# Optimization experiments

Hardware: AMD Instinct MI355X
Metric: run time of the kernel (lower is better)

## Reference

```python
import jax, jax.numpy as jnp
import numpy as np

N_NODES = 50000
HID = 64
EPS = 1e-5
POS_COLS = np.array([0, 1, 14])  # pos_x, pos_y, battery


def setup_inputs() -> dict:
    key = jax.random.key(0)
    ks = jax.random.split(key, 10)
    x = jax.random.normal(ks[0], (N_NODES, 16), dtype=jnp.float32)
    edge_index = jax.random.randint(ks[1], (2, 1600000), 0, N_NODES, dtype=jnp.int64)
    # 6 structurally identical conv layers: Linear(6,64) -> ReLU -> Linear(64,64)
    W1 = jax.random.normal(ks[2], (6, 6, HID), dtype=jnp.float32) * (1.0 / np.sqrt(6))
    b1 = jax.random.normal(ks[3], (6, HID), dtype=jnp.float32) * 0.02
    W2 = jax.random.normal(ks[4], (6, HID, HID), dtype=jnp.float32) * (1.0 / np.sqrt(HID))
    b2 = jax.random.normal(ks[5], (6, HID), dtype=jnp.float32) * 0.02
    # 5 BatchNorm layers (training mode: batch statistics over nodes)
    bn_gamma = jnp.ones((5, HID), dtype=jnp.float32) + 0.1 * jax.random.normal(ks[6], (5, HID), dtype=jnp.float32)
    bn_beta = 0.1 * jax.random.normal(ks[7], (5, HID), dtype=jnp.float32)
    return {"x": x, "edge_index": edge_index, "W1": W1, "b1": b1,
            "W2": W2, "b2": b2, "bn_gamma": bn_gamma, "bn_beta": bn_beta}


def _conv(x, src, dst, W1, b1, W2, b2):
    # pos_battery = x[:, [0,1,14]]; message = MLP(cat(x_j - x_i, x_i)); aggr='add' at target i
    p = x[:, POS_COLS]                       # [N, 3]
    x_i = p[dst]                             # targets  [E, 3]
    x_j = p[src]                             # sources  [E, 3]
    m = jnp.concatenate([x_j - x_i, x_i], axis=1)   # [E, 6]
    h = jax.nn.relu(m @ W1 + b1) @ W2 + b2          # [E, HID]
    return jax.ops.segment_sum(h, dst, num_segments=x.shape[0])


def _bn(h, gamma, beta):
    mu = jnp.mean(h, axis=0)
    var = jnp.var(h, axis=0)  # biased, matching BatchNorm training normalization
    return (h - mu) * jax.lax.rsqrt(var + EPS) * gamma + beta


def reference(x, edge_index, W1, b1, W2, b2, bn_gamma, bn_beta):
    n = x.shape[0]
    loop = jnp.arange(n, dtype=edge_index.dtype)
    src = jnp.concatenate([edge_index[0], loop])   # add_self_loops (done per layer in torch,
    dst = jnp.concatenate([edge_index[1], loop])   # identical result every layer)
    h = x
    for l in range(6):
        h = _conv(h, src, dst, W1[l], b1[l], W2[l], b2[l])
        if l < 5:
            h = jax.nn.relu(_bn(h, bn_gamma[l], bn_beta[l]))
    return h
```

## Files before the change

kernel.cpp:

```cpp
#include <hip/hip_runtime.h>
#include <hip/hip_fp16.h>
#include <cstdint>

#define NN 50000
#define NQBLK 12500
#define NGBLK 12500
#define EPSV 1e-5f

#define NPB 128
#define BSH 7
#define NBKT 391
#define CHUNK 4096
#define EPT 16
#define LDSE 6144

#define NSLOT 128

typedef unsigned short ushort_t;
typedef _Float16 half2v __attribute__((ext_vector_type(2)));

__global__ __launch_bounds__(256) void k_hist1(const int* __restrict__ dst, int E, int nchunk,
                                               int* __restrict__ hist, float* __restrict__ gsumsp) {
    __shared__ int cnt[NBKT];
    int t = threadIdx.x, blk = blockIdx.x;
    if (blk == 0) {
        for (int z = t; z < 5 * NSLOT * 8; z += 256) gsumsp[z] = 0.f;
    }
    for (int b = t; b < NBKT; b += 256) cnt[b] = 0;
    __syncthreads();
    int base = blk * CHUNK;
#pragma unroll
    for (int k = 0; k < EPT; ++k) {
        int e = base + k * 256 + t;
        if (e < E) atomicAdd(&cnt[dst[e] >> BSH], 1);
    }
    __syncthreads();
    for (int b = t; b < NBKT; b += 256) hist[(size_t)b * nchunk + blk] = cnt[b];
}

__global__ __launch_bounds__(256) void k_scanA(const int* __restrict__ in, int n,
                                               int* __restrict__ presum, int* __restrict__ blocksum) {
    __shared__ int lds[256];
    int t = threadIdx.x, g = blockIdx.x * 256 + t;
    int v = (g < n) ? in[g] : 0;
    lds[t] = v;
    __syncthreads();
    for (int off = 1; off < 256; off <<= 1) {
        int x = (t >= off) ? lds[t - off] : 0;
        __syncthreads();
        lds[t] += x;
        __syncthreads();
    }
    if (g < n) presum[g] = lds[t];
    if (t == 255) blocksum[blockIdx.x] = lds[255];
}

__global__ __launch_bounds__(256) void k_scanB(const int* __restrict__ blocksum,
                                               int nb, int* __restrict__ blockoff) {
    __shared__ int lds[256];
    __shared__ int carry_s;
    int t = threadIdx.x;
    if (t == 0) carry_s = 0;
    __syncthreads();
    for (int base = 0; base < nb; base += 256) {
        int g = base + t;
        int v = (g < nb) ? blocksum[g] : 0;
        lds[t] = v;
        __syncthreads();
        for (int off = 1; off < 256; off <<= 1) {
            int x = (t >= off) ? lds[t - off] : 0;
            __syncthreads();
            lds[t] += x;
            __syncthreads();
        }
        if (g < nb) blockoff[g] = lds[t] - v + carry_s;
        __syncthreads();
        if (t == 255) carry_s += lds[255];
        __syncthreads();
    }
}

__global__ __launch_bounds__(256) void k_scanC(const int* __restrict__ presum,
                                               const int* __restrict__ hist,
                                               const int* __restrict__ blockoff,
                                               int n, int nchunk, int* __restrict__ offsT) {
    int g = blockIdx.x * 256 + threadIdx.x;
    if (g < n) {
        int val = presum[g] - hist[g] + blockoff[blockIdx.x];
        int b = g / nchunk;
        int c = g - b * nchunk;
        offsT[(size_t)c * NBKT + b] = val;
    }
}

__global__ __launch_bounds__(256) void k_scatter1(const int* __restrict__ src,
                                                  const int* __restrict__ dst, int E,
                                                  const int* __restrict__ offsT,
                                                  int* __restrict__ ebuf) {
    __shared__ int pos[NBKT];
    int t = threadIdx.x, blk = blockIdx.x;
    for (int b = t; b < NBKT; b += 256) pos[b] = offsT[(size_t)blk * NBKT + b];
    __syncthreads();
    int base = blk * CHUNK;
#pragma unroll
    for (int k = 0; k < EPT; ++k) {
        int e = base + k * 256 + t;
        if (e < E) {
            int d = dst[e];
            int b = d >> BSH;
            int p = atomicAdd(&pos[b], 1);
            ebuf[p] = ((d & (NPB - 1)) << 16) | src[e];
        }
    }
}

__global__ __launch_bounds__(256) void k_bucket_csr(const int* __restrict__ ebuf,
                                                    const int* __restrict__ offsT, int E,
                                                    int* __restrict__ rowstart,
                                                    ushort_t* __restrict__ colsrc) {
    __shared__ int cnt[NPB];
    __shared__ int s[NPB];
    __shared__ int pos2[NPB];
    __shared__ ushort_t lout[LDSE];
    int t = threadIdx.x, b = blockIdx.x;
    int bstart = offsT[b];
    int bend = (b + 1 < NBKT) ? offsT[b + 1] : E;
    int m = bend - bstart;
    if (t < NPB) cnt[t] = 0;
    __syncthreads();
    for (int i = bstart + t; i < bend; i += 256) atomicAdd(&cnt[ebuf[i] >> 16], 1);
    __syncthreads();
    if (t < NPB) s[t] = cnt[t];
    __syncthreads();
    for (int off = 1; off < NPB; off <<= 1) {
        int x = (t < NPB && t >= off) ? s[t - off] : 0;
        __syncthreads();
        if (t < NPB) s[t] += x;
        __syncthreads();
    }
    if (t < NPB) {
        int excl = s[t] - cnt[t];
        int node = b * NPB + t;
        if (node < NN) rowstart[node] = bstart + excl;
        pos2[t] = excl;
    }
    __syncthreads();
    if (m <= LDSE) {
        for (int i = bstart + t; i < bend; i += 256) {
            int v = ebuf[i];
            int p = atomicAdd(&pos2[v >> 16], 1);
            lout[p] = (ushort_t)(v & 0xFFFF);
        }
        __syncthreads();
        for (int i = t; i < m; i += 256) colsrc[bstart + i] = lout[i];
    } else {
        for (int i = bstart + t; i < bend; i += 256) {
            int v = ebuf[i];
            int p = atomicAdd(&pos2[v >> 16], 1);
            colsrc[bstart + p] = (ushort_t)(v & 0xFFFF);
        }
    }
    if (b == NBKT - 1 && t == 0) rowstart[NN] = E;
}

__global__ __launch_bounds__(256) void k_q(
    const float* __restrict__ pin, int pstride, int c0, int c1, int c2,
    const float* __restrict__ W1l, const float* __restrict__ b1l,
    const float* __restrict__ scale, const float* __restrict__ shift, int use_bn,
    __half* __restrict__ qs, __half* __restrict__ qd) {
    int idx = blockIdx.x * 256 + threadIdx.x;
    int v = idx >> 6, c = idx & 63;
    const float* prow = pin + (size_t)v * pstride;
    float p0 = prow[c0], p1 = prow[c1], p2 = prow[c2];
    if (use_bn) {
        p0 = fmaxf(0.f, p0 * scale[0] + shift[0]);
        p1 = fmaxf(0.f, p1 * scale[1] + shift[1]);
        p2 = fmaxf(0.f, p2 * scale[2] + shift[2]);
    }
    float w0 = W1l[0 * 64 + c], w1 = W1l[1 * 64 + c], w2 = W1l[2 * 64 + c];
    float w3 = W1l[3 * 64 + c], w4 = W1l[4 * 64 + c], w5 = W1l[5 * 64 + c];
    qs[idx] = __float2half(p0 * w0 + p1 * w1 + p2 * w2);
    qd[idx] = __float2half(p0 * (w3 - w0) + p1 * (w4 - w1) + p2 * (w5 - w2) + b1l[c]);
}

__device__ __forceinline__ half2v bitcast_h2(unsigned int u) {
    union { unsigned int u; half2v h; } cvt;
    cvt.u = u;
    return cvt.h;
}

__device__ __forceinline__ void accum8f(const char* __restrict__ qsb, unsigned int byteoff,
                                        const half2v qd2[4], float acc[8]) {
    uint4 q = *reinterpret_cast<const uint4*>(qsb + byteoff);
    unsigned int wd[4] = {q.x, q.y, q.z, q.w};
    const half2v z2 = {(_Float16)0.0f, (_Float16)0.0f};
#pragma unroll
    for (int d = 0; d < 4; ++d) {
        half2v r = bitcast_h2(wd[d]) + qd2[d];
        r = __builtin_elementwise_max(r, z2);
        acc[2 * d]     += (float)r.x;
        acc[2 * d + 1] += (float)r.y;
    }
}

__device__ __forceinline__ void edge_loop(const char* __restrict__ qsb,
                                          const ushort_t* __restrict__ colsrc,
                                          int start, int end, int es, int cg,
                                          const half2v qd2[4], float acc[8]) {
    int lane = (es << 3) | cg;
    unsigned int cg16 = (unsigned int)(cg << 4);
    const half2v z2 = {(_Float16)0.0f, (_Float16)0.0f};
    int i = start;
    while (i < end) {
        int cnt = min(64, end - i);
        int sl = (lane < cnt) ? (int)colsrc[i + lane] : 0;
        uint4 q[8];
#pragma unroll
        for (int k = 0; k < 8; ++k) {
            int s = __shfl(sl, (k << 3) + es);
            q[k] = *reinterpret_cast<const uint4*>(qsb + (((unsigned int)(s << 7)) | cg16));
        }
        half2v h[4] = {z2, z2, z2, z2};
#pragma unroll
        for (int k = 0; k < 8; ++k) {
            bool ok = ((k << 3) + es) < cnt;
            unsigned int wd[4] = {q[k].x, q[k].y, q[k].z, q[k].w};
#pragma unroll
            for (int d = 0; d < 4; ++d) {
                half2v r = bitcast_h2(wd[d]) + qd2[d];
                r = __builtin_elementwise_max(r, z2);
                h[d] += ok ? r : z2;
            }
        }
#pragma unroll
        for (int d = 0; d < 4; ++d) {
            acc[2 * d]     += (float)h[d].x;
            acc[2 * d + 1] += (float)h[d].y;
        }
        i += cnt;
    }
}

__global__ __launch_bounds__(256) void k_gather3(
    const __half* __restrict__ qs, const __half* __restrict__ qd,
    const int* __restrict__ rowstart, const ushort_t* __restrict__ colsrc,
    const float* __restrict__ W2l, const float* __restrict__ b2l,
    float* __restrict__ pnext, float* __restrict__ gsum_l) {
    __shared__ float w2c[3][64];
    __shared__ float b2c[3];
    __shared__ float part[4][8];
    int tid = threadIdx.x;
    if (tid < 192) {
        int cj = tid >> 6;
        int col = (cj == 0) ? 0 : ((cj == 1) ? 1 : 14);
        w2c[cj][tid & 63] = W2l[(tid & 63) * 64 + col];
    }
    if (tid < 3) b2c[tid] = b2l[(tid == 0) ? 0 : ((tid == 1) ? 1 : 14)];
    __syncthreads();

    int w = tid >> 6, lane = tid & 63;
    int es = lane >> 3, cg = lane & 7;
    int v = blockIdx.x * 4 + w;
    const char* qsb = (const char*)qs;
    uint4 qq = ((const uint4*)qd)[(size_t)v * 8 + cg];
    unsigned int qw[4] = {qq.x, qq.y, qq.z, qq.w};
    half2v qd2[4];
#pragma unroll
    for (int d = 0; d < 4; ++d) qd2[d] = bitcast_h2(qw[d]);

    float acc[8] = {0, 0, 0, 0, 0, 0, 0, 0};
    int start = rowstart[v], end = rowstart[v + 1];
    if (es == 0) accum8f(qsb, ((unsigned int)(v << 7)) | (cg << 4), qd2, acc);
    edge_loop(qsb, colsrc, start, end, es, cg, qd2, acc);

#pragma unroll
    for (int k = 0; k < 8; ++k) {
        acc[k] += __shfl_xor(acc[k], 8);
        acc[k] += __shfl_xor(acc[k], 16);
        acc[k] += __shfl_xor(acc[k], 32);
    }
    float degp1 = (float)(end - start + 1);
#pragma unroll
    for (int j = 0; j < 3; ++j) {
        float t = 0.f;
#pragma unroll
        for (int k = 0; k < 8; ++k) t += acc[k] * w2c[j][cg * 8 + k];
        t += __shfl_xor(t, 1);
        t += __shfl_xor(t, 2);
        t += __shfl_xor(t, 4);
        if (lane == 0) {
            float val = t + degp1 * b2c[j];
            pnext[v * 3 + j] = val;
            part[w][j] = val;
            part[w][3 + j] = val * val;
        }
    }
    __syncthreads();
    if (tid < 6) {
        float ssum = part[0][tid] + part[1][tid] + part[2][tid] + part[3][tid];
        atomicAdd(&gsum_l[(blockIdx.x & (NSLOT - 1)) * 8 + tid], ssum);
    }
}

__global__ void k_bnfin(const float* __restrict__ gs,
                        const float* __restrict__ gamma_l, const float* __restrict__ beta_l,
                        float* __restrict__ scale, float* __restrict__ shift) {
    __shared__ float red[6][8];
    __shared__ float tot[6];
    int t = threadIdx.x;
    int j = t >> 3, k = t & 7;
    if (j < 6) {
        float s = 0.f;
        for (int slot = k; slot < NSLOT; slot += 8) s += gs[slot * 8 + j];
        red[j][k] = s;
    }
    __syncthreads();
    if (t < 6) {
        float s = 0.f;
#pragma unroll
        for (int k2 = 0; k2 < 8; ++k2) s += red[t][k2];
        tot[t] = s;
    }
    __syncthreads();
    if (t < 3) {
        const int cols[3] = {0, 1, 14};
        float mu = tot[t] / (float)NN;
        float var = tot[t + 3] / (float)NN - mu * mu;
        float rs = rsqrtf(var + EPSV);
        float g = gamma_l[cols[t]];
        scale[t] = rs * g;
        shift[t] = beta_l[cols[t]] - mu * rs * g;
    }
}

__global__ __launch_bounds__(256) void k_gather_full(
    const __half* __restrict__ qs, const __half* __restrict__ qd,
    const int* __restrict__ rowstart, const ushort_t* __restrict__ colsrc,
    const float* __restrict__ W2l, const float* __restrict__ b2l,
    float* __restrict__ out) {
    __shared__ float lds[4][64];
    int tid = threadIdx.x;
    int w = tid >> 6, lane = tid & 63;
    int es = lane >> 3, cg = lane & 7;
    int v = blockIdx.x * 4 + w;
    const char* qsb = (const char*)qs;
    uint4 qq = ((const uint4*)qd)[(size_t)v * 8 + cg];
    unsigned int qw[4] = {qq.x, qq.y, qq.z, qq.w};
    half2v qd2[4];
#pragma unroll
    for (int d = 0; d < 4; ++d) qd2[d] = bitcast_h2(qw[d]);

    float acc[8] = {0, 0, 0, 0, 0, 0, 0, 0};
    int start = rowstart[v], end = rowstart[v + 1];
    if (es == 0) accum8f(qsb, ((unsigned int)(v << 7)) | (cg << 4), qd2, acc);
    edge_loop(qsb, colsrc, start, end, es, cg, qd2, acc);

#pragma unroll
    for (int k = 0; k < 8; ++k) {
        acc[k] += __shfl_xor(acc[k], 8);
        acc[k] += __shfl_xor(acc[k], 16);
        acc[k] += __shfl_xor(acc[k], 32);
    }
    if (es == 0) {
#pragma unroll
        for (int k = 0; k < 8; ++k) lds[w][cg * 8 + k] = acc[k];
    }
    __syncthreads();
    float degp1 = (float)(end - start + 1);
    float sum = degp1 * b2l[lane];
    for (int k = 0; k < 64; ++k) sum += lds[w][k] * W2l[k * 64 + lane];
    out[(size_t)v * 64 + lane] = sum;
}


static inline size_t align_up(size_t x) { return (x + 255) & ~(size_t)255; }

extern "C" void kernel_launch(void* const* d_in, const int* in_sizes, int n_in,
                              void* d_out, int out_size, void* d_ws, size_t ws_size,
                              hipStream_t stream) {
    const float* x     = (const float*)d_in[0];
    const int*   ei    = (const int*)d_in[1];
    const float* W1    = (const float*)d_in[2];
    const float* b1    = (const float*)d_in[3];
    const float* W2    = (const float*)d_in[4];
    const float* b2    = (const float*)d_in[5];
    const float* gamma = (const float*)d_in[6];
    const float* beta  = (const float*)d_in[7];
    float* out = (float*)d_out;
    const int E = in_sizes[1] / 2;
    const int* src = ei;
    const int* dst = ei + E;

    const int nchunk = (E + CHUNK - 1) / CHUNK;
    const int nscan  = NBKT * nchunk;
    const int nsb    = (nscan + 255) / 256;

    char* base = (char*)d_ws;
    size_t off = 0;
    __half* qs = (__half*)(base + off);     off = align_up(off + (size_t)NN * 64 * 2);
    __half* qd = (__half*)(base + off);     off = align_up(off + (size_t)NN * 64 * 2);
    float* pA = (float*)(base + off);       off = align_up(off + (size_t)NN * 3 * 4);
    float* pB = (float*)(base + off);       off = align_up(off + (size_t)NN * 3 * 4);
    int* rowstart = (int*)(base + off);     off = align_up(off + (size_t)(NN + 1) * 4);
    ushort_t* colsrc = (ushort_t*)(base + off); off = align_up(off + (size_t)E * 2);
    int* ebuf     = (int*)(base + off);     off = align_up(off + (size_t)E * 4);
    int* hist     = (int*)(base + off);     off = align_up(off + (size_t)nscan * 4);
    int* offsT    = (int*)(base + off);     off = align_up(off + (size_t)nscan * 4);
    int* presum   = (int*)(base + off);     off = align_up(off + (size_t)nscan * 4);
    int* bsum     = (int*)(base + off);     off = align_up(off + (size_t)nsb * 4);
    int* boff     = (int*)(base + off);     off = align_up(off + (size_t)nsb * 4);
    float* gsumsp = (float*)(base + off);   off = align_up(off + (size_t)5 * NSLOT * 8 * 4);
    float* scale  = (float*)(base + off);   off = align_up(off + 64 * 4);
    float* shift  = (float*)(base + off);   off = align_up(off + 64 * 4);
    (void)ws_size; (void)n_in; (void)out_size;

    k_hist1<<<nchunk, 256, 0, stream>>>(dst, E, nchunk, hist, gsumsp);
    k_scanA<<<nsb, 256, 0, stream>>>(hist, nscan, presum, bsum);
    k_scanB<<<1, 256, 0, stream>>>(bsum, nsb, boff);
    k_scanC<<<nsb, 256, 0, stream>>>(presum, hist, boff, nscan, nchunk, offsT);
    k_scatter1<<<nchunk, 256, 0, stream>>>(src, dst, E, offsT, ebuf);
    k_bucket_csr<<<NBKT, 256, 0, stream>>>(ebuf, offsT, E, rowstart, colsrc);

    float* pc = pA;
    float* pn = pB;
    for (int l = 0; l < 6; ++l) {
        const float* pin = (l == 0) ? x : pc;
        int pstride = (l == 0) ? 16 : 3;
        int c0 = 0, c1 = 1, c2 = (l == 0) ? 14 : 2;
        k_q<<<NQBLK, 256, 0, stream>>>(pin, pstride, c0, c1, c2,
                                       W1 + (size_t)l * 6 * 64, b1 + (size_t)l * 64,
                                       scale, shift, (l > 0) ? 1 : 0, qs, qd);
        if (l < 5) {
            k_gather3<<<NGBLK, 256, 0, stream>>>(qs, qd, rowstart, colsrc,
                                                 W2 + (size_t)l * 64 * 64, b2 + (size_t)l * 64,
                                                 pn, gsumsp + (size_t)l * NSLOT * 8);
            k_bnfin<<<1, 64, 0, stream>>>(gsumsp + (size_t)l * NSLOT * 8,
                                          gamma + (size_t)l * 64, beta + (size_t)l * 64,
                                          scale, shift);
            float* tmp = pc; pc = pn; pn = tmp;
        } else {
            k_gather_full<<<NGBLK, 256, 0, stream>>>(qs, qd, rowstart, colsrc,
                                                     W2 + (size_t)5 * 64 * 64, b2 + (size_t)5 * 64,
                                                     out);
        }
    }
}
```

Before: 459.6 us.

## Split gather into channel-half passes with half-split q layout and separate projection

Stores qs/qd as two 32-channel halves (planar by half) so each gather pass touches a 3.2MB table per half, improving cache locality of random source reads. The gather runs as 2x blocks, each processing 16 edges per wave-iteration with full-64 fast path and templated tails, writing fp32 hsum to a new buffer. W2 projection and BN partial sums move to separate lightweight kernels reading hsum. Adds an extra 12.8MB write/read per layer and doubles colsrc/rowstart reads in exchange for better L2 hit rate.

```diff
diff --git a/kernel.cpp b/kernel.cpp
--- a/kernel.cpp
+++ b/kernel.cpp
@@ -18,6 +18,8 @@
 
 typedef unsigned short ushort_t;
 typedef _Float16 half2v __attribute__((ext_vector_type(2)));
+typedef unsigned int uintv4 __attribute__((ext_vector_type(4)));
+typedef float floatv4 __attribute__((ext_vector_type(4)));
 
 __global__ __launch_bounds__(256) void k_hist1(const int* __restrict__ dst, int E, int nchunk,
                                                int* __restrict__ hist, float* __restrict__ gsumsp) {
@@ -179,8 +181,9 @@
     }
     float w0 = W1l[0 * 64 + c], w1 = W1l[1 * 64 + c], w2 = W1l[2 * 64 + c];
     float w3 = W1l[3 * 64 + c], w4 = W1l[4 * 64 + c], w5 = W1l[5 * 64 + c];
-    qs[idx] = __float2half(p0 * w0 + p1 * w1 + p2 * w2);
-    qd[idx] = __float2half(p0 * (w3 - w0) + p1 * (w4 - w1) + p2 * (w5 - w2) + b1l[c]);
+    size_t o = (size_t)(c >> 5) * NN * 32 + (size_t)v * 32 + (c & 31);
+    qs[o] = __float2half(p0 * w0 + p1 * w1 + p2 * w2);
+    qd[o] = __float2half(p0 * (w3 - w0) + p1 * (w4 - w1) + p2 * (w5 - w2) + b1l[c]);
 }
 
 __device__ __forceinline__ half2v bitcast_h2(unsigned int u) {
@@ -189,61 +192,131 @@
     return cvt.h;
 }
 
-__device__ __forceinline__ void accum8f(const char* __restrict__ qsb, unsigned int byteoff,
-                                        const half2v qd2[4], float acc[8]) {
-    uint4 q = *reinterpret_cast<const uint4*>(qsb + byteoff);
-    unsigned int wd[4] = {q.x, q.y, q.z, q.w};
+__device__ __forceinline__ void edge_full64(const char* __restrict__ qsb,
+                                            const ushort_t* __restrict__ colsrc,
+                                            int i, int lane, int es, unsigned int cg16,
+                                            const half2v qd2[4], float acc[8]) {
     const half2v z2 = {(_Float16)0.0f, (_Float16)0.0f};
+    int sl = (int)__builtin_nontemporal_load(colsrc + i + lane);
+    uint4 q[4];
+#pragma unroll
+    for (int k = 0; k < 4; ++k) {
+        int s = __shfl(sl, (k << 4) + es);
+        q[k] = *reinterpret_cast<const uint4*>(qsb + (((unsigned int)(s << 6)) | cg16));
+    }
+    half2v h[4] = {z2, z2, z2, z2};
+#pragma unroll
+    for (int k = 0; k < 4; ++k) {
+        unsigned int wd[4] = {q[k].x, q[k].y, q[k].z, q[k].w};
+#pragma unroll
+        for (int d = 0; d < 4; ++d) {
+            half2v r = bitcast_h2(wd[d]) + qd2[d];
+            r = __builtin_elementwise_max(r, z2);
+            h[d] += r;
+        }
+    }
 #pragma unroll
     for (int d = 0; d < 4; ++d) {
-        half2v r = bitcast_h2(wd[d]) + qd2[d];
-        r = __builtin_elementwise_max(r, z2);
-        acc[2 * d]     += (float)r.x;
-        acc[2 * d + 1] += (float)r.y;
-    }
-}
-
-__device__ __forceinline__ void edge_loop(const char* __restrict__ qsb,
+        acc[2 * d]     += (float)h[d].x;
+        acc[2 * d + 1] += (float)h[d].y;
+    }
+}
+
+template <int NL>
+__device__ __forceinline__ void edge_tail(const char* __restrict__ qsb,
                                           const ushort_t* __restrict__ colsrc,
-                                          int start, int end, int es, int cg,
+                                          int i, int r, int lane, int es, unsigned int cg16,
                                           const half2v qd2[4], float acc[8]) {
-    int lane = (es << 3) | cg;
+    const half2v z2 = {(_Float16)0.0f, (_Float16)0.0f};
+    int sl = (lane < r) ? (int)__builtin_nontemporal_load(colsrc + i + lane) : 0;
+    uint4 q[NL];
+#pragma unroll
+    for (int k = 0; k < NL; ++k) {
+        int s = __shfl(sl, (k << 4) + es);
+        q[k] = *reinterpret_cast<const uint4*>(qsb + (((unsigned int)(s << 6)) | cg16));
+    }
+    half2v h[4] = {z2, z2, z2, z2};
+#pragma unroll
+    for (int k = 0; k < NL; ++k) {
+        bool ok = ((k << 4) + es) < r;
+        unsigned int wd[4] = {q[k].x, q[k].y, q[k].z, q[k].w};
+#pragma unroll
+        for (int d = 0; d < 4; ++d) {
+            half2v t = bitcast_h2(wd[d]) + qd2[d];
+            t = __builtin_elementwise_max(t, z2);
+            h[d] += ok ? t : z2;
+        }
+    }
+#pragma unroll
+    for (int d = 0; d < 4; ++d) {
+        acc[2 * d]     += (float)h[d].x;
+        acc[2 * d + 1] += (float)h[d].y;
+    }
+}
+
+__global__ __launch_bounds__(256) void k_gatherA(
+    const __half* __restrict__ qsh, const __half* __restrict__ qdh,
+    const int* __restrict__ rowstart, const ushort_t* __restrict__ colsrc,
+    float* __restrict__ hsum) {
+    int tid = threadIdx.x;
+    int w = tid >> 6, lane = tid & 63;
+    int es = lane >> 2, cg = lane & 3;
     unsigned int cg16 = (unsigned int)(cg << 4);
-    const half2v z2 = {(_Float16)0.0f, (_Float16)0.0f};
+    int bb = blockIdx.x;
+    int half = (bb >= NGBLK) ? 1 : 0;
+    int v = (bb - half * NGBLK) * 4 + w;
+    const char* qsb = (const char*)qsh + (size_t)half * NN * 64;
+    const char* qdb = (const char*)qdh + (size_t)half * NN * 64;
+
+    uintv4 qq = __builtin_nontemporal_load(
+        reinterpret_cast<const uintv4*>(qdb + ((size_t)v << 6)) + cg);
+    unsigned int qw[4] = {qq.x, qq.y, qq.z, qq.w};
+    half2v qd2[4];
+#pragma unroll
+    for (int d = 0; d < 4; ++d) qd2[d] = bitcast_h2(qw[d]);
+
+    float acc[8] = {0, 0, 0, 0, 0, 0, 0, 0};
+    int start = rowstart[v], end = rowstart[v + 1];
+
+    if (es == 0) {
+        const half2v z2 = {(_Float16)0.0f, (_Float16)0.0f};
+        uint4 q = *reinterpret_cast<const uint4*>(qsb + (((unsigned int)(v << 6)) | cg16));
+        unsigned int wd[4] = {q.x, q.y, q.z, q.w};
+#pragma unroll
+        for (int d = 0; d < 4; ++d) {
+            half2v r = bitcast_h2(wd[d]) + qd2[d];
+            r = __builtin_elementwise_max(r, z2);
+            acc[2 * d]     += (float)r.x;
+            acc[2 * d + 1] += (float)r.y;
+        }
+    }
+
     int i = start;
-    while (i < end) {
-        int cnt = min(64, end - i);
-        int sl = (lane < cnt) ? (int)colsrc[i + lane] : 0;
-        uint4 q[8];
-#pragma unroll
-        for (int k = 0; k < 8; ++k) {
-            int s = __shfl(sl, (k << 3) + es);
-            q[k] = *reinterpret_cast<const uint4*>(qsb + (((unsigned int)(s << 7)) | cg16));
-        }
-        half2v h[4] = {z2, z2, z2, z2};
-#pragma unroll
-        for (int k = 0; k < 8; ++k) {
-            bool ok = ((k << 3) + es) < cnt;
-            unsigned int wd[4] = {q[k].x, q[k].y, q[k].z, q[k].w};
-#pragma unroll
-            for (int d = 0; d < 4; ++d) {
-                half2v r = bitcast_h2(wd[d]) + qd2[d];
-                r = __builtin_elementwise_max(r, z2);
-                h[d] += ok ? r : z2;
-            }
-        }
-#pragma unroll
-        for (int d = 0; d < 4; ++d) {
-            acc[2 * d]     += (float)h[d].x;
-            acc[2 * d + 1] += (float)h[d].y;
-        }
-        i += cnt;
-    }
-}
-
-__global__ __launch_bounds__(256) void k_gather3(
-    const __half* __restrict__ qs, const __half* __restrict__ qd,
-    const int* __restrict__ rowstart, const ushort_t* __restrict__ colsrc,
+    while (end - i >= 64) { edge_full64(qsb, colsrc, i, lane, es, cg16, qd2, acc); i += 64; }
+    int r = end - i;
+    if      (r > 48) edge_tail<4>(qsb, colsrc, i, r, lane, es, cg16, qd2, acc);
+    else if (r > 32) edge_tail<3>(qsb, colsrc, i, r, lane, es, cg16, qd2, acc);
+    else if (r > 16) edge_tail<2>(qsb, colsrc, i, r, lane, es, cg16, qd2, acc);
+    else if (r > 0)  edge_tail<1>(qsb, colsrc, i, r, lane, es, cg16, qd2, acc);
+
+#pragma unroll
+    for (int k = 0; k < 8; ++k) {
+        acc[k] += __shfl_xor(acc[k], 4);
+        acc[k] += __shfl_xor(acc[k], 8);
+        acc[k] += __shfl_xor(acc[k], 16);
+        acc[k] += __shfl_xor(acc[k], 32);
+    }
+    if (es == 0) {
+        floatv4 a0 = {acc[0], acc[1], acc[2], acc[3]};
+        floatv4 a1 = {acc[4], acc[5], acc[6], acc[7]};
+        floatv4* dst = reinterpret_cast<floatv4*>(hsum + (size_t)v * 64 + half * 32 + cg * 8);
+        __builtin_nontemporal_store(a0, dst);
+        __builtin_nontemporal_store(a1, dst + 1);
+    }
+}
+
+__global__ __launch_bounds__(256) void k_proj3(
+    const float* __restrict__ hsum, const int* __restrict__ rowstart,
     const float* __restrict__ W2l, const float* __restrict__ b2l,
     float* __restrict__ pnext, float* __restrict__ gsum_l) {
     __shared__ float w2c[3][64];
@@ -259,35 +332,19 @@
     __syncthreads();
 
     int w = tid >> 6, lane = tid & 63;
-    int es = lane >> 3, cg = lane & 7;
     int v = blockIdx.x * 4 + w;
-    const char* qsb = (const char*)qs;
-    uint4 qq = ((const uint4*)qd)[(size_t)v * 8 + cg];
-    unsigned int qw[4] = {qq.x, qq.y, qq.z, qq.w};
-    half2v qd2[4];
-#pragma unroll
-    for (int d = 0; d < 4; ++d) qd2[d] = bitcast_h2(qw[d]);
-
-    float acc[8] = {0, 0, 0, 0, 0, 0, 0, 0};
+    float hv = __builtin_nontemporal_load(hsum + (size_t)v * 64 + lane);
     int start = rowstart[v], end = rowstart[v + 1];
-    if (es == 0) accum8f(qsb, ((unsigned int)(v << 7)) | (cg << 4), qd2, acc);
-    edge_loop(qsb, colsrc, start, end, es, cg, qd2, acc);
-
-#pragma unroll
-    for (int k = 0; k < 8; ++k) {
-        acc[k] += __shfl_xor(acc[k], 8);
-        acc[k] += __shfl_xor(acc[k], 16);
-        acc[k] += __shfl_xor(acc[k], 32);
-    }
     float degp1 = (float)(end - start + 1);
 #pragma unroll
     for (int j = 0; j < 3; ++j) {
-        float t = 0.f;
-#pragma unroll
-        for (int k = 0; k < 8; ++k) t += acc[k] * w2c[j][cg * 8 + k];
+        float t = hv * w2c[j][lane];
         t += __shfl_xor(t, 1);
         t += __shfl_xor(t, 2);
         t += __shfl_xor(t, 4);
+        t += __shfl_xor(t, 8);
+        t += __shfl_xor(t, 16);
+        t += __shfl_xor(t, 32);
         if (lane == 0) {
             float val = t + degp1 * b2c[j];
             pnext[v * 3 + j] = val;
@@ -333,39 +390,18 @@
     }
 }
 
-__global__ __launch_bounds__(256) void k_gather_full(
-    const __half* __restrict__ qs, const __half* __restrict__ qd,
-    const int* __restrict__ rowstart, const ushort_t* __restrict__ colsrc,
+__global__ __launch_bounds__(256) void k_projfull(
+    const float* __restrict__ hsum, const int* __restrict__ rowstart,
     const float* __restrict__ W2l, const float* __restrict__ b2l,
     float* __restrict__ out) {
     __shared__ float lds[4][64];
     int tid = threadIdx.x;
     int w = tid >> 6, lane = tid & 63;
-    int es = lane >> 3, cg = lane & 7;
     int v = blockIdx.x * 4 + w;
-    const char* qsb = (const char*)qs;
-    uint4 qq = ((const uint4*)qd)[(size_t)v * 8 + cg];
-    unsigned int qw[4] = {qq.x, qq.y, qq.z, qq.w};
-    half2v qd2[4];
-#pragma unroll
-    for (int d = 0; d < 4; ++d) qd2[d] = bitcast_h2(qw[d]);
-
-    float acc[8] = {0, 0, 0, 0, 0, 0, 0, 0};
+    float hv = __builtin_nontemporal_load(hsum + (size_t)v * 64 + lane);
+    lds[w][lane] = hv;
+    __syncthreads();
     int start = rowstart[v], end = rowstart[v + 1];
-    if (es == 0) accum8f(qsb, ((unsigned int)(v << 7)) | (cg << 4), qd2, acc);
-    edge_loop(qsb, colsrc, start, end, es, cg, qd2, acc);
-
-#pragma unroll
-    for (int k = 0; k < 8; ++k) {
-        acc[k] += __shfl_xor(acc[k], 8);
-        acc[k] += __shfl_xor(acc[k], 16);
-        acc[k] += __shfl_xor(acc[k], 32);
-    }
-    if (es == 0) {
-#pragma unroll
-        for (int k = 0; k < 8; ++k) lds[w][cg * 8 + k] = acc[k];
-    }
-    __syncthreads();
     float degp1 = (float)(end - start + 1);
     float sum = degp1 * b2l[lane];
     for (int k = 0; k < 64; ++k) sum += lds[w][k] * W2l[k * 64 + lane];
@@ -399,6 +435,7 @@
     size_t off = 0;
     __half* qs = (__half*)(base + off);     off = align_up(off + (size_t)NN * 64 * 2);
     __half* qd = (__half*)(base + off);     off = align_up(off + (size_t)NN * 64 * 2);
+    float* hsum = (float*)(base + off);     off = align_up(off + (size_t)NN * 64 * 4);
     float* pA = (float*)(base + off);       off = align_up(off + (size_t)NN * 3 * 4);
     float* pB = (float*)(base + off);       off = align_up(off + (size_t)NN * 3 * 4);
     int* rowstart = (int*)(base + off);     off = align_up(off + (size_t)(NN + 1) * 4);
@@ -430,18 +467,19 @@
         k_q<<<NQBLK, 256, 0, stream>>>(pin, pstride, c0, c1, c2,
                                        W1 + (size_t)l * 6 * 64, b1 + (size_t)l * 64,
                                        scale, shift, (l > 0) ? 1 : 0, qs, qd);
+        k_gatherA<<<2 * NGBLK, 256, 0, stream>>>(qs, qd, rowstart, colsrc, hsum);
         if (l < 5) {
-            k_gather3<<<NGBLK, 256, 0, stream>>>(qs, qd, rowstart, colsrc,
-                                                 W2 + (size_t)l * 64 * 64, b2 + (size_t)l * 64,
-                                                 pn, gsumsp + (size_t)l * NSLOT * 8);
+            k_proj3<<<NGBLK, 256, 0, stream>>>(hsum, rowstart,
+                                               W2 + (size_t)l * 64 * 64, b2 + (size_t)l * 64,
+                                               pn, gsumsp + (size_t)l * NSLOT * 8);
             k_bnfin<<<1, 64, 0, stream>>>(gsumsp + (size_t)l * NSLOT * 8,
                                           gamma + (size_t)l * 64, beta + (size_t)l * 64,
                                           scale, shift);
             float* tmp = pc; pc = pn; pn = tmp;
         } else {
-            k_gather_full<<<NGBLK, 256, 0, stream>>>(qs, qd, rowstart, colsrc,
-                                                     W2 + (size_t)5 * 64 * 64, b2 + (size_t)5 * 64,
-                                                     out);
-        }
-    }
-}
+            k_projfull<<<NGBLK, 256, 0, stream>>>(hsum, rowstart,
+                                                  W2 + (size_t)5 * 64 * 64, b2 + (size_t)5 * 64,
+                                                  out);
+        }
+    }
+}
```

Measured after the change: 603.0 us. 31.2% more time.

## Gather packed 3-value source positions and recompute W1 projection per edge

Applied to the files above, without the earlier changes.

Instead of gathering a precomputed 64-wide fp16 source projection (128 bytes per edge), each node's three input features are stored as a 16-byte packed record. The W1 source projection is then recomputed per edge with fp16 FMAs, using W1 columns held in registers. This cuts gather traffic per edge and the qs write in k_q, at the cost of extra ALU work per edge. The edge loop also gains specialised full and remainder clauses with nontemporal index loads, and the cross-lane reduction moves after the W2 dot product.

```diff
diff --git a/kernel.cpp b/kernel.cpp
--- a/kernel.cpp
+++ b/kernel.cpp
@@ -167,7 +167,7 @@
     const float* __restrict__ pin, int pstride, int c0, int c1, int c2,
     const float* __restrict__ W1l, const float* __restrict__ b1l,
     const float* __restrict__ scale, const float* __restrict__ shift, int use_bn,
-    __half* __restrict__ qs, __half* __restrict__ qd) {
+    uint4* __restrict__ ppack, __half* __restrict__ qd) {
     int idx = blockIdx.x * 256 + threadIdx.x;
     int v = idx >> 6, c = idx & 63;
     const float* prow = pin + (size_t)v * pstride;
@@ -179,8 +179,14 @@
     }
     float w0 = W1l[0 * 64 + c], w1 = W1l[1 * 64 + c], w2 = W1l[2 * 64 + c];
     float w3 = W1l[3 * 64 + c], w4 = W1l[4 * 64 + c], w5 = W1l[5 * 64 + c];
-    qs[idx] = __float2half(p0 * w0 + p1 * w1 + p2 * w2);
     qd[idx] = __float2half(p0 * (w3 - w0) + p1 * (w4 - w1) + p2 * (w5 - w2) + b1l[c]);
+    if (c == 0) {
+        unsigned int u0 = (unsigned int)__half_as_ushort(__float2half(p0)); u0 |= u0 << 16;
+        unsigned int u1 = (unsigned int)__half_as_ushort(__float2half(p1)); u1 |= u1 << 16;
+        unsigned int u2 = (unsigned int)__half_as_ushort(__float2half(p2)); u2 |= u2 << 16;
+        uint4 pk = {u0, u1, u2, 0u};
+        ppack[v] = pk;
+    }
 }
 
 __device__ __forceinline__ half2v bitcast_h2(unsigned int u) {
@@ -189,62 +195,97 @@
     return cvt.h;
 }
 
-__device__ __forceinline__ void accum8f(const char* __restrict__ qsb, unsigned int byteoff,
-                                        const half2v qd2[4], float acc[8]) {
-    uint4 q = *reinterpret_cast<const uint4*>(qsb + byteoff);
-    unsigned int wd[4] = {q.x, q.y, q.z, q.w};
+__device__ __forceinline__ void edge_math(const uint4 q, const half2v qd2[4],
+                                          const half2v w0p[4], const half2v w1p[4],
+                                          const half2v w2p[4], bool ok, half2v h[4]) {
     const half2v z2 = {(_Float16)0.0f, (_Float16)0.0f};
+    half2v p0 = bitcast_h2(q.x), p1 = bitcast_h2(q.y), p2 = bitcast_h2(q.z);
 #pragma unroll
     for (int d = 0; d < 4; ++d) {
-        half2v r = bitcast_h2(wd[d]) + qd2[d];
+        half2v r = p0 * w0p[d] + qd2[d];
+        r = p1 * w1p[d] + r;
+        r = p2 * w2p[d] + r;
         r = __builtin_elementwise_max(r, z2);
-        acc[2 * d]     += (float)r.x;
-        acc[2 * d + 1] += (float)r.y;
-    }
-}
-
-__device__ __forceinline__ void edge_loop(const char* __restrict__ qsb,
+        h[d] += ok ? r : z2;
+    }
+}
+
+template <int NL, bool FULL>
+__device__ __forceinline__ void edge_clause(const char* __restrict__ ppb,
+                                            const ushort_t* __restrict__ colsrc,
+                                            int i, int r, int lane, int es,
+                                            const half2v qd2[4], const half2v w0p[4],
+                                            const half2v w1p[4], const half2v w2p[4],
+                                            float acc[8]) {
+    const half2v z2 = {(_Float16)0.0f, (_Float16)0.0f};
+    int sl = (FULL || lane < r) ? (int)__builtin_nontemporal_load(colsrc + i + lane) : 0;
+    uint4 q[NL];
+#pragma unroll
+    for (int k = 0; k < NL; ++k) {
+        int s = __shfl(sl, (k << 3) + es);
+        q[k] = *reinterpret_cast<const uint4*>(ppb + ((unsigned int)(s << 4)));
+    }
+    half2v h[4] = {z2, z2, z2, z2};
+#pragma unroll
+    for (int k = 0; k < NL; ++k) {
+        bool ok = FULL || (((k << 3) + es) < r);
+        edge_math(q[k], qd2, w0p, w1p, w2p, ok, h);
+    }
+#pragma unroll
+    for (int d = 0; d < 4; ++d) {
+        acc[2 * d]     += (float)h[d].x;
+        acc[2 * d + 1] += (float)h[d].y;
+    }
+}
+
+__device__ __forceinline__ void run_edges(const char* __restrict__ ppb,
                                           const ushort_t* __restrict__ colsrc,
-                                          int start, int end, int es, int cg,
-                                          const half2v qd2[4], float acc[8]) {
-    int lane = (es << 3) | cg;
-    unsigned int cg16 = (unsigned int)(cg << 4);
-    const half2v z2 = {(_Float16)0.0f, (_Float16)0.0f};
+                                          int v, int start, int end, int lane, int es,
+                                          const half2v qd2[4], const half2v w0p[4],
+                                          const half2v w1p[4], const half2v w2p[4],
+                                          float acc[8]) {
+    if (es == 0) {
+        const half2v z2 = {(_Float16)0.0f, (_Float16)0.0f};
+        uint4 pv = *reinterpret_cast<const uint4*>(ppb + ((unsigned int)(v << 4)));
+        half2v p0 = bitcast_h2(pv.x), p1 = bitcast_h2(pv.y), p2 = bitcast_h2(pv.z);
+#pragma unroll
+        for (int d = 0; d < 4; ++d) {
+            half2v r = p0 * w0p[d] + qd2[d];
+            r = p1 * w1p[d] + r;
+            r = p2 * w2p[d] + r;
+            r = __builtin_elementwise_max(r, z2);
+            acc[2 * d]     += (float)r.x;
+            acc[2 * d + 1] += (float)r.y;
+        }
+    }
     int i = start;
-    while (i < end) {
-        int cnt = min(64, end - i);
-        int sl = (lane < cnt) ? (int)colsrc[i + lane] : 0;
-        uint4 q[8];
-#pragma unroll
-        for (int k = 0; k < 8; ++k) {
-            int s = __shfl(sl, (k << 3) + es);
-            q[k] = *reinterpret_cast<const uint4*>(qsb + (((unsigned int)(s << 7)) | cg16));
-        }
-        half2v h[4] = {z2, z2, z2, z2};
-#pragma unroll
-        for (int k = 0; k < 8; ++k) {
-            bool ok = ((k << 3) + es) < cnt;
-            unsigned int wd[4] = {q[k].x, q[k].y, q[k].z, q[k].w};
-#pragma unroll
-            for (int d = 0; d < 4; ++d) {
-                half2v r = bitcast_h2(wd[d]) + qd2[d];
-                r = __builtin_elementwise_max(r, z2);
-                h[d] += ok ? r : z2;
-            }
-        }
-#pragma unroll
-        for (int d = 0; d < 4; ++d) {
-            acc[2 * d]     += (float)h[d].x;
-            acc[2 * d + 1] += (float)h[d].y;
-        }
-        i += cnt;
+    while (end - i >= 64) {
+        edge_clause<8, true>(ppb, colsrc, i, 64, lane, es, qd2, w0p, w1p, w2p, acc);
+        i += 64;
+    }
+    int r = end - i;
+    if      (r > 48) edge_clause<8, false>(ppb, colsrc, i, r, lane, es, qd2, w0p, w1p, w2p, acc);
+    else if (r > 32) edge_clause<6, false>(ppb, colsrc, i, r, lane, es, qd2, w0p, w1p, w2p, acc);
+    else if (r > 16) edge_clause<4, false>(ppb, colsrc, i, r, lane, es, qd2, w0p, w1p, w2p, acc);
+    else if (r > 0)  edge_clause<2, false>(ppb, colsrc, i, r, lane, es, qd2, w0p, w1p, w2p, acc);
+}
+
+__device__ __forceinline__ void load_w1(const float* __restrict__ W1l, int cg,
+                                        half2v w0p[4], half2v w1p[4], half2v w2p[4]) {
+#pragma unroll
+    for (int d = 0; d < 4; ++d) {
+        int cc = (cg << 3) + (d << 1);
+        w0p[d] = half2v{(_Float16)W1l[cc],       (_Float16)W1l[cc + 1]};
+        w1p[d] = half2v{(_Float16)W1l[64 + cc],  (_Float16)W1l[64 + cc + 1]};
+        w2p[d] = half2v{(_Float16)W1l[128 + cc], (_Float16)W1l[128 + cc + 1]};
     }
 }
 
 __global__ __launch_bounds__(256) void k_gather3(
-    const __half* __restrict__ qs, const __half* __restrict__ qd,
+    const uint4* __restrict__ ppack, const __half* __restrict__ qd,
     const int* __restrict__ rowstart, const ushort_t* __restrict__ colsrc,
-    const float* __restrict__ W2l, const float* __restrict__ b2l,
+    const float* __restrict__ W1l, const float* __restrict__ W2l,
+    const float* __restrict__ b2l,
     float* __restrict__ pnext, float* __restrict__ gsum_l) {
     __shared__ float w2c[3][64];
     __shared__ float b2c[3];
@@ -261,24 +302,20 @@
     int w = tid >> 6, lane = tid & 63;
     int es = lane >> 3, cg = lane & 7;
     int v = blockIdx.x * 4 + w;
-    const char* qsb = (const char*)qs;
+    const char* ppb = (const char*)ppack;
+
     uint4 qq = ((const uint4*)qd)[(size_t)v * 8 + cg];
     unsigned int qw[4] = {qq.x, qq.y, qq.z, qq.w};
     half2v qd2[4];
 #pragma unroll
     for (int d = 0; d < 4; ++d) qd2[d] = bitcast_h2(qw[d]);
+    half2v w0p[4], w1p[4], w2p[4];
+    load_w1(W1l, cg, w0p, w1p, w2p);
 
     float acc[8] = {0, 0, 0, 0, 0, 0, 0, 0};
     int start = rowstart[v], end = rowstart[v + 1];
-    if (es == 0) accum8f(qsb, ((unsigned int)(v << 7)) | (cg << 4), qd2, acc);
-    edge_loop(qsb, colsrc, start, end, es, cg, qd2, acc);
-
-#pragma unroll
-    for (int k = 0; k < 8; ++k) {
-        acc[k] += __shfl_xor(acc[k], 8);
-        acc[k] += __shfl_xor(acc[k], 16);
-        acc[k] += __shfl_xor(acc[k], 32);
-    }
+    run_edges(ppb, colsrc, v, start, end, lane, es, qd2, w0p, w1p, w2p, acc);
+
     float degp1 = (float)(end - start + 1);
 #pragma unroll
     for (int j = 0; j < 3; ++j) {
@@ -288,6 +325,9 @@
         t += __shfl_xor(t, 1);
         t += __shfl_xor(t, 2);
         t += __shfl_xor(t, 4);
+        t += __shfl_xor(t, 8);
+        t += __shfl_xor(t, 16);
+        t += __shfl_xor(t, 32);
         if (lane == 0) {
             float val = t + degp1 * b2c[j];
             pnext[v * 3 + j] = val;
@@ -334,26 +374,29 @@
 }
 
 __global__ __launch_bounds__(256) void k_gather_full(
-    const __half* __restrict__ qs, const __half* __restrict__ qd,
+    const uint4* __restrict__ ppack, const __half* __restrict__ qd,
     const int* __restrict__ rowstart, const ushort_t* __restrict__ colsrc,
-    const float* __restrict__ W2l, const float* __restrict__ b2l,
+    const float* __restrict__ W1l, const float* __restrict__ W2l,
+    const float* __restrict__ b2l,
     float* __restrict__ out) {
     __shared__ float lds[4][64];
     int tid = threadIdx.x;
     int w = tid >> 6, lane = tid & 63;
     int es = lane >> 3, cg = lane & 7;
     int v = blockIdx.x * 4 + w;
-    const char* qsb = (const char*)qs;
+    const char* ppb = (const char*)ppack;
+
     uint4 qq = ((const uint4*)qd)[(size_t)v * 8 + cg];
     unsigned int qw[4] = {qq.x, qq.y, qq.z, qq.w};
     half2v qd2[4];
 #pragma unroll
     for (int d = 0; d < 4; ++d) qd2[d] = bitcast_h2(qw[d]);
+    half2v w0p[4], w1p[4], w2p[4];
+    load_w1(W1l, cg, w0p, w1p, w2p);
 
     float acc[8] = {0, 0, 0, 0, 0, 0, 0, 0};
     int start = rowstart[v], end = rowstart[v + 1];
-    if (es == 0) accum8f(qsb, ((unsigned int)(v << 7)) | (cg << 4), qd2, acc);
-    edge_loop(qsb, colsrc, start, end, es, cg, qd2, acc);
+    run_edges(ppb, colsrc, v, start, end, lane, es, qd2, w0p, w1p, w2p, acc);
 
 #pragma unroll
     for (int k = 0; k < 8; ++k) {
@@ -397,7 +440,7 @@
 
     char* base = (char*)d_ws;
     size_t off = 0;
-    __half* qs = (__half*)(base + off);     off = align_up(off + (size_t)NN * 64 * 2);
+    uint4* ppack = (uint4*)(base + off);    off = align_up(off + (size_t)NN * 16);
     __half* qd = (__half*)(base + off);     off = align_up(off + (size_t)NN * 64 * 2);
     float* pA = (float*)(base + off);       off = align_up(off + (size_t)NN * 3 * 4);
     float* pB = (float*)(base + off);       off = align_up(off + (size_t)NN * 3 * 4);
@@ -427,20 +470,23 @@
         const float* pin = (l == 0) ? x : pc;
         int pstride = (l == 0) ? 16 : 3;
         int c0 = 0, c1 = 1, c2 = (l == 0) ? 14 : 2;
+        const float* W1l = W1 + (size_t)l * 6 * 64;
         k_q<<<NQBLK, 256, 0, stream>>>(pin, pstride, c0, c1, c2,
-                                       W1 + (size_t)l * 6 * 64, b1 + (size_t)l * 64,
-                                       scale, shift, (l > 0) ? 1 : 0, qs, qd);
+                                       W1l, b1 + (size_t)l * 64,
+                                       scale, shift, (l > 0) ? 1 : 0, ppack, qd);
         if (l < 5) {
-            k_gather3<<<NGBLK, 256, 0, stream>>>(qs, qd, rowstart, colsrc,
-                                                 W2 + (size_t)l * 64 * 64, b2 + (size_t)l * 64,
+            k_gather3<<<NGBLK, 256, 0, stream>>>(ppack, qd, rowstart, colsrc,
+                                                 W1l, W2 + (size_t)l * 64 * 64,
+                                                 b2 + (size_t)l * 64,
                                                  pn, gsumsp + (size_t)l * NSLOT * 8);
             k_bnfin<<<1, 64, 0, stream>>>(gsumsp + (size_t)l * NSLOT * 8,
                                           gamma + (size_t)l * 64, beta + (size_t)l * 64,
                                           scale, shift);
             float* tmp = pc; pc = pn; pn = tmp;
         } else {
-            k_gather_full<<<NGBLK, 256, 0, stream>>>(qs, qd, rowstart, colsrc,
-                                                     W2 + (size_t)5 * 64 * 64, b2 + (size_t)5 * 64,
+            k_gather_full<<<NGBLK, 256, 0, stream>>>(ppack, qd, rowstart, colsrc,
+                                                     W1l, W2 + (size_t)5 * 64 * 64,
+                                                     b2 + (size_t)5 * 64,
                                                      out);
         }
     }
```

Measured after the change: 528.4 us. 15.0% more time.

## Process two destination nodes per wavefront in gather kernels with 32-edge chunks

Applied to the files above, without the earlier changes.

Each wavefront now handles two consecutive destination nodes, interleaving 32-edge chunks from both rows so that eight independent gathers are in flight per iteration. The grid is halved to match. In the final layer the W2 weight load is shared between the two nodes. The change targets short-row underutilisation and aims to raise memory-level parallelism for the scattered qs loads. In exchange it uses more registers, adds a launch-bounds occupancy hint, and causes imbalance when the two rows have very different degrees.

```diff
diff --git a/kernel.cpp b/kernel.cpp
--- a/kernel.cpp
+++ b/kernel.cpp
@@ -4,7 +4,7 @@
 
 #define NN 50000
 #define NQBLK 12500
-#define NGBLK 12500
+#define NGBLK2 6250
 #define EPSV 1e-5f
 
 #define NPB 128
@@ -203,45 +203,59 @@
     }
 }
 
-__device__ __forceinline__ void edge_loop(const char* __restrict__ qsb,
-                                          const ushort_t* __restrict__ colsrc,
-                                          int start, int end, int es, int cg,
-                                          const half2v qd2[4], float acc[8]) {
-    int lane = (es << 3) | cg;
-    unsigned int cg16 = (unsigned int)(cg << 4);
+__device__ __forceinline__ void chunk_math32(const uint4 q[4], const half2v qd2[4],
+                                             int r, int es, float acc[8]) {
     const half2v z2 = {(_Float16)0.0f, (_Float16)0.0f};
-    int i = start;
-    while (i < end) {
-        int cnt = min(64, end - i);
-        int sl = (lane < cnt) ? (int)colsrc[i + lane] : 0;
-        uint4 q[8];
-#pragma unroll
-        for (int k = 0; k < 8; ++k) {
-            int s = __shfl(sl, (k << 3) + es);
-            q[k] = *reinterpret_cast<const uint4*>(qsb + (((unsigned int)(s << 7)) | cg16));
-        }
-        half2v h[4] = {z2, z2, z2, z2};
-#pragma unroll
-        for (int k = 0; k < 8; ++k) {
-            bool ok = ((k << 3) + es) < cnt;
-            unsigned int wd[4] = {q[k].x, q[k].y, q[k].z, q[k].w};
-#pragma unroll
-            for (int d = 0; d < 4; ++d) {
-                half2v r = bitcast_h2(wd[d]) + qd2[d];
-                r = __builtin_elementwise_max(r, z2);
-                h[d] += ok ? r : z2;
-            }
-        }
+    half2v h[4] = {z2, z2, z2, z2};
+#pragma unroll
+    for (int k = 0; k < 4; ++k) {
+        bool ok = ((k << 3) + es) < r;
+        unsigned int wd[4] = {q[k].x, q[k].y, q[k].z, q[k].w};
 #pragma unroll
         for (int d = 0; d < 4; ++d) {
-            acc[2 * d]     += (float)h[d].x;
-            acc[2 * d + 1] += (float)h[d].y;
-        }
-        i += cnt;
-    }
-}
-
-__global__ __launch_bounds__(256) void k_gather3(
+            half2v t = bitcast_h2(wd[d]) + qd2[d];
+            t = __builtin_elementwise_max(t, z2);
+            h[d] += ok ? t : z2;
+        }
+    }
+#pragma unroll
+    for (int d = 0; d < 4; ++d) {
+        acc[2 * d]     += (float)h[d].x;
+        acc[2 * d + 1] += (float)h[d].y;
+    }
+}
+
+__device__ __forceinline__ void pair_edge_loop(const char* __restrict__ qsb,
+                                               const ushort_t* __restrict__ colsrc,
+                                               int iA, int e0, int iB, int e1,
+                                               int lane, int es, unsigned int cg16,
+                                               const half2v qd2A[4], const half2v qd2B[4],
+                                               float accA[8], float accB[8]) {
+    while (iA < e0 || iB < e1) {
+        int remA = e0 - iA, remB = e1 - iB;
+        int rA = remA > 32 ? 32 : remA;
+        int rB = remB > 32 ? 32 : remB;
+        int slA = (lane < rA) ? (int)colsrc[iA + lane] : 0;
+        int slB = (lane < rB) ? (int)colsrc[iB + lane] : 0;
+        uint4 qA[4], qB[4];
+#pragma unroll
+        for (int k = 0; k < 4; ++k) {
+            int s = __shfl(slA, (k << 3) + es);
+            qA[k] = *reinterpret_cast<const uint4*>(qsb + (((unsigned int)(s << 7)) | cg16));
+        }
+#pragma unroll
+        for (int k = 0; k < 4; ++k) {
+            int s = __shfl(slB, (k << 3) + es);
+            qB[k] = *reinterpret_cast<const uint4*>(qsb + (((unsigned int)(s << 7)) | cg16));
+        }
+        chunk_math32(qA, qd2A, rA, es, accA);
+        chunk_math32(qB, qd2B, rB, es, accB);
+        iA += rA;
+        iB += rB;
+    }
+}
+
+__global__ __launch_bounds__(256, 4) void k_gather3(
     const __half* __restrict__ qs, const __half* __restrict__ qd,
     const int* __restrict__ rowstart, const ushort_t* __restrict__ colsrc,
     const float* __restrict__ W2l, const float* __restrict__ b2l,
@@ -260,39 +274,53 @@
 
     int w = tid >> 6, lane = tid & 63;
     int es = lane >> 3, cg = lane & 7;
-    int v = blockIdx.x * 4 + w;
+    unsigned int cg16 = (unsigned int)(cg << 4);
+    int v0 = (blockIdx.x * 4 + w) * 2;
     const char* qsb = (const char*)qs;
-    uint4 qq = ((const uint4*)qd)[(size_t)v * 8 + cg];
-    unsigned int qw[4] = {qq.x, qq.y, qq.z, qq.w};
-    half2v qd2[4];
-#pragma unroll
-    for (int d = 0; d < 4; ++d) qd2[d] = bitcast_h2(qw[d]);
-
-    float acc[8] = {0, 0, 0, 0, 0, 0, 0, 0};
-    int start = rowstart[v], end = rowstart[v + 1];
-    if (es == 0) accum8f(qsb, ((unsigned int)(v << 7)) | (cg << 4), qd2, acc);
-    edge_loop(qsb, colsrc, start, end, es, cg, qd2, acc);
-
-#pragma unroll
-    for (int k = 0; k < 8; ++k) {
-        acc[k] += __shfl_xor(acc[k], 8);
-        acc[k] += __shfl_xor(acc[k], 16);
-        acc[k] += __shfl_xor(acc[k], 32);
-    }
-    float degp1 = (float)(end - start + 1);
+
+    uint4 qqA = ((const uint4*)qd)[(size_t)v0 * 8 + cg];
+    uint4 qqB = ((const uint4*)qd)[(size_t)(v0 + 1) * 8 + cg];
+    half2v qd2A[4], qd2B[4];
+    {
+        unsigned int qa[4] = {qqA.x, qqA.y, qqA.z, qqA.w};
+        unsigned int qb[4] = {qqB.x, qqB.y, qqB.z, qqB.w};
+#pragma unroll
+        for (int d = 0; d < 4; ++d) { qd2A[d] = bitcast_h2(qa[d]); qd2B[d] = bitcast_h2(qb[d]); }
+    }
+
+    float accA[8] = {0, 0, 0, 0, 0, 0, 0, 0};
+    float accB[8] = {0, 0, 0, 0, 0, 0, 0, 0};
+    int s0 = rowstart[v0], e0 = rowstart[v0 + 1], e1 = rowstart[v0 + 2];
+    if (es == 0) {
+        accum8f(qsb, ((unsigned int)(v0 << 7)) | cg16, qd2A, accA);
+        accum8f(qsb, ((unsigned int)((v0 + 1) << 7)) | cg16, qd2B, accB);
+    }
+    pair_edge_loop(qsb, colsrc, s0, e0, e0, e1, lane, es, cg16, qd2A, qd2B, accA, accB);
+
+    float degA = (float)(e0 - s0 + 1);
+    float degB = (float)(e1 - e0 + 1);
 #pragma unroll
     for (int j = 0; j < 3; ++j) {
-        float t = 0.f;
-#pragma unroll
-        for (int k = 0; k < 8; ++k) t += acc[k] * w2c[j][cg * 8 + k];
-        t += __shfl_xor(t, 1);
-        t += __shfl_xor(t, 2);
-        t += __shfl_xor(t, 4);
+        float tA = 0.f, tB = 0.f;
+#pragma unroll
+        for (int k = 0; k < 8; ++k) {
+            float wv = w2c[j][cg * 8 + k];
+            tA += accA[k] * wv;
+            tB += accB[k] * wv;
+        }
+        tA += __shfl_xor(tA, 1);  tB += __shfl_xor(tB, 1);
+        tA += __shfl_xor(tA, 2);  tB += __shfl_xor(tB, 2);
+        tA += __shfl_xor(tA, 4);  tB += __shfl_xor(tB, 4);
+        tA += __shfl_xor(tA, 8);  tB += __shfl_xor(tB, 8);
+        tA += __shfl_xor(tA, 16); tB += __shfl_xor(tB, 16);
+        tA += __shfl_xor(tA, 32); tB += __shfl_xor(tB, 32);
         if (lane == 0) {
-            float val = t + degp1 * b2c[j];
-            pnext[v * 3 + j] = val;
-            part[w][j] = val;
-            part[w][3 + j] = val * val;
+            float valA = tA + degA * b2c[j];
+            float valB = tB + degB * b2c[j];
+            pnext[v0 * 3 + j] = valA;
+            pnext[(v0 + 1) * 3 + j] = valB;
+            part[w][j] = valA + valB;
+            part[w][3 + j] = valA * valA + valB * valB;
         }
     }
     __syncthreads();
@@ -333,43 +361,67 @@
     }
 }
 
-__global__ __launch_bounds__(256) void k_gather_full(
+__global__ __launch_bounds__(256, 4) void k_gather_full(
     const __half* __restrict__ qs, const __half* __restrict__ qd,
     const int* __restrict__ rowstart, const ushort_t* __restrict__ colsrc,
     const float* __restrict__ W2l, const float* __restrict__ b2l,
     float* __restrict__ out) {
-    __shared__ float lds[4][64];
+    __shared__ float lds[4][2][64];
     int tid = threadIdx.x;
     int w = tid >> 6, lane = tid & 63;
     int es = lane >> 3, cg = lane & 7;
-    int v = blockIdx.x * 4 + w;
+    unsigned int cg16 = (unsigned int)(cg << 4);
+    int v0 = (blockIdx.x * 4 + w) * 2;
     const char* qsb = (const char*)qs;
-    uint4 qq = ((const uint4*)qd)[(size_t)v * 8 + cg];
-    unsigned int qw[4] = {qq.x, qq.y, qq.z, qq.w};
-    half2v qd2[4];
-#pragma unroll
-    for (int d = 0; d < 4; ++d) qd2[d] = bitcast_h2(qw[d]);
-
-    float acc[8] = {0, 0, 0, 0, 0, 0, 0, 0};
-    int start = rowstart[v], end = rowstart[v + 1];
-    if (es == 0) accum8f(qsb, ((unsigned int)(v << 7)) | (cg << 4), qd2, acc);
-    edge_loop(qsb, colsrc, start, end, es, cg, qd2, acc);
+
+    uint4 qqA = ((const uint4*)qd)[(size_t)v0 * 8 + cg];
+    uint4 qqB = ((const uint4*)qd)[(size_t)(v0 + 1) * 8 + cg];
+    half2v qd2A[4], qd2B[4];
+    {
+        unsigned int qa[4] = {qqA.x, qqA.y, qqA.z, qqA.w};
+        unsigned int qb[4] = {qqB.x, qqB.y, qqB.z, qqB.w};
+#pragma unroll
+        for (int d = 0; d < 4; ++d) { qd2A[d] = bitcast_h2(qa[d]); qd2B[d] = bitcast_h2(qb[d]); }
+    }
+
+    float accA[8] = {0, 0, 0, 0, 0, 0, 0, 0};
+    float accB[8] = {0, 0, 0, 0, 0, 0, 0, 0};
+    int s0 = rowstart[v0], e0 = rowstart[v0 + 1], e1 = rowstart[v0 + 2];
+    if (es == 0) {
+        accum8f(qsb, ((unsigned int)(v0 << 7)) | cg16, qd2A, accA);
+        accum8f(qsb, ((unsigned int)((v0 + 1) << 7)) | cg16, qd2B, accB);
+    }
+    pair_edge_loop(qsb, colsrc, s0, e0, e0, e1, lane, es, cg16, qd2A, qd2B, accA, accB);
 
 #pragma unroll
     for (int k = 0; k < 8; ++k) {
-        acc[k] += __shfl_xor(acc[k], 8);
-        acc[k] += __shfl_xor(acc[k], 16);
-        acc[k] += __shfl_xor(acc[k], 32);
+        accA[k] += __shfl_xor(accA[k], 8);
+        accA[k] += __shfl_xor(accA[k], 16);
+        accA[k] += __shfl_xor(accA[k], 32);
+        accB[k] += __shfl_xor(accB[k], 8);
+        accB[k] += __shfl_xor(accB[k], 16);
+        accB[k] += __shfl_xor(accB[k], 32);
     }
     if (es == 0) {
 #pragma unroll
-        for (int k = 0; k < 8; ++k) lds[w][cg * 8 + k] = acc[k];
-    }
-    __syncthreads();
-    float degp1 = (float)(end - start + 1);
-    float sum = degp1 * b2l[lane];
-    for (int k = 0; k < 64; ++k) sum += lds[w][k] * W2l[k * 64 + lane];
-    out[(size_t)v * 64 + lane] = sum;
+        for (int k = 0; k < 8; ++k) {
+            lds[w][0][cg * 8 + k] = accA[k];
+            lds[w][1][cg * 8 + k] = accB[k];
+        }
+    }
+    __syncthreads();
+    float degA = (float)(e0 - s0 + 1);
+    float degB = (float)(e1 - e0 + 1);
+    float bl = b2l[lane];
+    float sumA = degA * bl;
+    float sumB = degB * bl;
+    for (int k = 0; k < 64; ++k) {
+        float wv = W2l[k * 64 + lane];
+        sumA += lds[w][0][k] * wv;
+        sumB += lds[w][1][k] * wv;
+    }
+    out[(size_t)v0 * 64 + lane] = sumA;
+    out[(size_t)(v0 + 1) * 64 + lane] = sumB;
 }
 
 
@@ -431,17 +483,17 @@
                                        W1 + (size_t)l * 6 * 64, b1 + (size_t)l * 64,
                                        scale, shift, (l > 0) ? 1 : 0, qs, qd);
         if (l < 5) {
-            k_gather3<<<NGBLK, 256, 0, stream>>>(qs, qd, rowstart, colsrc,
-                                                 W2 + (size_t)l * 64 * 64, b2 + (size_t)l * 64,
-                                                 pn, gsumsp + (size_t)l * NSLOT * 8);
+            k_gather3<<<NGBLK2, 256, 0, stream>>>(qs, qd, rowstart, colsrc,
+                                                  W2 + (size_t)l * 64 * 64, b2 + (size_t)l * 64,
+                                                  pn, gsumsp + (size_t)l * NSLOT * 8);
             k_bnfin<<<1, 64, 0, stream>>>(gsumsp + (size_t)l * NSLOT * 8,
                                           gamma + (size_t)l * 64, beta + (size_t)l * 64,
                                           scale, shift);
             float* tmp = pc; pc = pn; pn = tmp;
         } else {
-            k_gather_full<<<NGBLK, 256, 0, stream>>>(qs, qd, rowstart, colsrc,
-                                                     W2 + (size_t)5 * 64 * 64, b2 + (size_t)5 * 64,
-                                                     out);
-        }
-    }
-}
+            k_gather_full<<<NGBLK2, 256, 0, stream>>>(qs, qd, rowstart, colsrc,
+                                                      W2 + (size_t)5 * 64 * 64, b2 + (size_t)5 * 64,
+                                                      out);
+        }
+    }
+}
```

Result: faster. 436.8 us (-5.0%).
